# Performance work log

Hardware: AMD Instinct MI355X
Metric: run time of the kernel (lower is better)

The kernel has to match this reference:

```python
import jax, jax.numpy as jnp
import numpy as np

LRELU_GAIN = 2.0 ** 0.5  # util.lrelu_gain (assumed sqrt(2))
EPS = 1e-8


def upsample2_bilinear_ac(x):
    # F.upsample_bilinear == bilinear with align_corners=True, scale 2
    B, C, H, W = x.shape
    def lerp_axis(t, n, axis):
        c = jnp.arange(2 * n, dtype=jnp.float32) * (n - 1) / (2 * n - 1)
        i0 = jnp.floor(c).astype(jnp.int32)
        i1 = jnp.minimum(i0 + 1, n - 1)
        f = c - i0.astype(jnp.float32)
        a = jnp.take(t, i0, axis=axis)
        b = jnp.take(t, i1, axis=axis)
        shape = [1] * t.ndim
        shape[axis] = 2 * n
        f = f.reshape(shape)
        return a * (1.0 - f) + b * f
    x = lerp_axis(x, H, 2)
    x = lerp_axis(x, W, 3)
    return x


def conv1x1(x, weight, bias, gain):
    # Conv2dNormalizedLR with kernel_size=1: he = gain/sqrt(in)
    cin = weight.shape[1]
    he = gain / float(cin) ** 0.5
    y = jnp.einsum('bihw,oi->bohw', x, weight[:, :, 0, 0] * he)
    return y + bias[None, :, None, None]


def mod_conv3x3(x, weight, style, gain):
    # weight: [Cin, Cout, 3, 3]; style: [B, Cin]
    cin, cout, k, _ = weight.shape
    he = gain / float(cin * k * k) ** 0.5
    wmod = style[:, :, None, None, None] * (weight * he)[None]  # [B,Cin,Cout,k,k]
    # demodulation: normalize over (in, kh, kw) per out channel
    d = jax.lax.rsqrt(jnp.sum(wmod * wmod, axis=(1, 3, 4), keepdims=True) + EPS)
    wmod = wmod * d
    # conv_transpose2d(stride=1, pad=1, k=3) == conv2d with transposed+flipped kernel, pad=1
    kern = jnp.flip(jnp.transpose(wmod, (0, 2, 1, 3, 4)), axis=(3, 4))  # [B,Cout,Cin,k,k]
    def one(xb, kb):
        return jax.lax.conv_general_dilated(
            xb[None], kb, (1, 1), ((1, 1), (1, 1)),
            dimension_numbers=('NCHW', 'OIHW', 'NCHW'))[0]
    y = jax.vmap(one)(x, kern)
    return y * gain


def noise_affine(noise, w_s, b_s, w_b, b_b):
    # Baff*: 1x1 conv from 1 channel, gain=1 -> he=1
    ys = noise * w_s[None, :, 0, None, 0, None][:, :, :, 0] if False else noise * w_s[:, 0, 0, 0][None, :, None, None] + b_s[None, :, None, None]
    yb = noise * w_b[:, 0, 0, 0][None, :, None, None] + b_b[None, :, None, None]
    return ys, yb


def block_forward(x, w, noise1, noise2, conv1_w, bias1, conv2_w, bias2,
                  Aaff1_w, Aaff1_b, Aaff2_w, Aaff2_b,
                  Baff1s_w, Baff1s_b, Baff1b_w, Baff1b_b,
                  Baff2s_w, Baff2s_b, Baff2b_w, Baff2b_b,
                  rgb_w, rgb_b):
    x = upsample2_bilinear_ac(x)
    style1 = conv1x1(w, Aaff1_w, Aaff1_b, 1.0)[:, :, 0, 0]  # [B, Cin]
    x = mod_conv3x3(x, conv1_w, style1, LRELU_GAIN)
    ys, yb = noise_affine(noise1, Baff1s_w, Baff1s_b, Baff1b_w, Baff1b_b)
    x = x * ys + yb + bias1
    x = jax.nn.leaky_relu(x, 0.2)
    style2 = conv1x1(w, Aaff2_w, Aaff2_b, 1.0)[:, :, 0, 0]
    x = mod_conv3x3(x, conv2_w, style2, LRELU_GAIN)
    ys, yb = noise_affine(noise2, Baff2s_w, Baff2s_b, Baff2b_w, Baff2b_b)
    x = x * ys + yb + bias2
    x = jax.nn.leaky_relu(x, 0.2)
    rgb = conv1x1(x, rgb_w, rgb_b, 0.03)
    return x, rgb


def setup_inputs() -> dict:
    key = jax.random.key(0)
    ks = jax.random.split(key, 20)
    B, Cin, Cout, Wd, H, W = 8, 512, 512, 512, 32, 32
    inp = {
        'x': jax.random.normal(ks[0], (B, Cin, H, W), jnp.float32),
        'w': jax.random.normal(ks[1], (B, Wd, 1, 1), jnp.float32),
        'noise1': jax.random.normal(ks[2], (B, 1, 2 * H, 2 * W), jnp.float32),
        'noise2': jax.random.normal(ks[3], (B, 1, 2 * H, 2 * W), jnp.float32),
        'conv1_w': jax.random.normal(ks[4], (Cin, Cout, 3, 3), jnp.float32),
        'bias1': jnp.zeros((1, Cout, 1, 1), jnp.float32),
        'conv2_w': jax.random.normal(ks[5], (Cout, Cout, 3, 3), jnp.float32),
        'bias2': jnp.zeros((1, Cout, 1, 1), jnp.float32),
        'Aaff1_w': jax.random.normal(ks[6], (Cin, Wd, 1, 1), jnp.float32),
        'Aaff1_b': jnp.zeros((Cin,), jnp.float32),
        'Aaff2_w': jax.random.normal(ks[7], (Cout, Wd, 1, 1), jnp.float32),
        'Aaff2_b': jnp.zeros((Cout,), jnp.float32),
        'Baff1s_w': jax.random.normal(ks[8], (Cout, 1, 1, 1), jnp.float32) * 0.1,
        'Baff1s_b': jnp.ones((Cout,), jnp.float32),
        'Baff1b_w': jax.random.normal(ks[9], (Cout, 1, 1, 1), jnp.float32) * 0.1,
        'Baff1b_b': jnp.zeros((Cout,), jnp.float32),
        'Baff2s_w': jax.random.normal(ks[10], (Cout, 1, 1, 1), jnp.float32) * 0.1,
        'Baff2s_b': jnp.ones((Cout,), jnp.float32),
        'Baff2b_w': jax.random.normal(ks[11], (Cout, 1, 1, 1), jnp.float32) * 0.1,
        'Baff2b_b': jnp.zeros((Cout,), jnp.float32),
        'rgb_w': jax.random.normal(ks[12], (3, Cout, 1, 1), jnp.float32),
        'rgb_b': jnp.zeros((3,), jnp.float32),
    }
    return inp


def reference(x, w, noise1, noise2, conv1_w, bias1, conv2_w, bias2,
              Aaff1_w, Aaff1_b, Aaff2_w, Aaff2_b,
              Baff1s_w, Baff1s_b, Baff1b_w, Baff1b_b,
              Baff2s_w, Baff2s_b, Baff2b_w, Baff2b_b,
              rgb_w, rgb_b):
    return block_forward(x, w, noise1, noise2, conv1_w, bias1, conv2_w, bias2,
                         Aaff1_w, Aaff1_b, Aaff2_w, Aaff2_b,
                         Baff1s_w, Baff1s_b, Baff1b_w, Baff1b_b,
                         Baff2s_w, Baff2s_b, Baff2b_w, Baff2b_b,
                         rgb_w, rgb_b)
```

## Files before the change

### kernel.cpp

```cpp
#include <hip/hip_runtime.h>
#include <hip/hip_bf16.h>

#define BB 8
#define CC 512
#define HO 64
#define HP 66
#define NPIX (BB*HO*HO)

typedef float f32x4 __attribute__((ext_vector_type(4)));
typedef __bf16 bf16x8 __attribute__((ext_vector_type(8)));
using bf16 = __hip_bfloat16;

__device__ __forceinline__ void gload16(const void* g, void* l) {
    __builtin_amdgcn_global_load_lds((const __attribute__((address_space(1))) void*)g,
                                     (__attribute__((address_space(3))) void*)l, 16, 0, 0);
}

__device__ __forceinline__ float waveRedSum(float v) {
    #pragma unroll
    for (int off = 32; off; off >>= 1) v += __shfl_down(v, off);
    return v;
}

__global__ void prep_weights(const float* __restrict__ Wsrc, float* __restrict__ S2ho,
                             bf16* __restrict__ keffT, float he) {
    int t = blockIdx.x * blockDim.x + threadIdx.x;
    int i = t & (CC-1), o = t >> 9;
    const float* wp = Wsrc + (i*CC + o)*9;
    float v[9]; float s2 = 0.f;
    #pragma unroll
    for (int k = 0; k < 9; ++k) { v[k] = wp[k] * he; s2 += v[k]*v[k]; }
    S2ho[o*CC + i] = s2;
    #pragma unroll
    for (int tp = 0; tp < 9; ++tp) keffT[(tp*CC + o)*CC + i] = (bf16)v[8 - tp];
}

__global__ void style_kernel(const float* __restrict__ w,
                             const float* __restrict__ A1, const float* __restrict__ A1b,
                             const float* __restrict__ A2, const float* __restrict__ A2b,
                             float* __restrict__ s1, float* __restrict__ s2) {
    int wid = (blockIdx.x * blockDim.x + threadIdx.x) >> 6;
    int lane = threadIdx.x & 63;
    int set = wid >= BB*CC; int rem = set ? wid - BB*CC : wid;
    int b = rem >> 9, i = rem & (CC-1);
    const float* A = set ? A2 : A1;
    const float* wb = w + b*CC;
    float sum = 0.f;
    for (int d = lane; d < CC; d += 64) sum += wb[d] * A[i*CC + d];
    sum = waveRedSum(sum);
    if (lane == 0) {
        float r = sum * 0.04419417382415922f + (set ? A2b : A1b)[i];
        (set ? s2 : s1)[b*CC + i] = r;
    }
}

__global__ void demod_kernel(const float* __restrict__ s1, const float* __restrict__ S21,
                             const float* __restrict__ s2, const float* __restrict__ S22,
                             float* __restrict__ dg1, float* __restrict__ dg2, float gain) {
    int wid = (blockIdx.x * blockDim.x + threadIdx.x) >> 6;
    int lane = threadIdx.x & 63;
    int set = wid >= BB*CC; int rem = set ? wid - BB*CC : wid;
    int b = rem >> 9, o = rem & (CC-1);
    const float* st = (set ? s2 : s1) + b*CC;
    const float* S2 = (set ? S22 : S21) + o*CC;
    float sum = 0.f;
    for (int i = lane; i < CC; i += 64) { float sv = st[i]; sum += sv*sv*S2[i]; }
    sum = waveRedSum(sum);
    if (lane == 0) (set ? dg2 : dg1)[b*CC + o] = gain * rsqrtf(sum + 1e-8f);
}

__global__ void upsample_mod(const float* __restrict__ x, const float* __restrict__ s1,
                             bf16* __restrict__ xs1) {
    __shared__ float usl[16][CC];
    int blk = blockIdx.x;
    int i = threadIdx.x;
    int b = blk >> 10, rem = blk & 1023, p = rem >> 4, q0 = (rem & 15) << 2;
    const float scale = 31.0f / 63.0f;
    float chf = p * scale; int h0 = (int)chf; float fh = chf - h0; int h1 = min(h0 + 1, 31);
    int wa = min(((int)(q0 * scale)) & ~3, 24);
    const float* xb = x + ((size_t)(b*CC + i) << 10);
    f32x4 r00 = *(const f32x4*)(xb + (h0 << 5) + wa);
    f32x4 r01 = *(const f32x4*)(xb + (h0 << 5) + wa + 4);
    f32x4 r10 = *(const f32x4*)(xb + (h1 << 5) + wa);
    f32x4 r11 = *(const f32x4*)(xb + (h1 << 5) + wa + 4);
    #pragma unroll
    for (int k = 0; k < 4; ++k) {
        usl[k][i] = r00[k]; usl[4 + k][i] = r01[k];
        usl[8 + k][i] = r10[k]; usl[12 + k][i] = r11[k];
    }
    float sv = s1[b*CC + i];
    #pragma unroll
    for (int dq = 0; dq < 4; ++dq) {
        int q = q0 + dq;
        float cwf = q * scale; int w0 = (int)cwf; float fw = cwf - w0;
        int i0 = w0 - wa, i1 = min(w0 + 1, 31) - wa;
        float v00 = usl[i0][i], v01 = usl[i1][i];
        float v10 = usl[8 + i0][i], v11 = usl[8 + i1][i];
        float va = v00*(1.f-fh) + v10*fh;
        float vb = v01*(1.f-fh) + v11*fh;
        float v  = (va*(1.f-fw) + vb*fw) * sv;
        xs1[(((b*HP) + p + 1)*HP + (q + 1))*CC + i] = (bf16)v;
    }
}

__global__ void halo_zero(bf16* __restrict__ xs1, bf16* __restrict__ xs2) {
    int blk = blockIdx.x;
    bf16* dst = (blk & 1) ? xs2 : xs1;
    int idx = blk >> 1;
    int b = idx / 260, rm = idx - b*260;
    int p, q;
    if (rm < 66)       { p = 0;        q = rm; }
    else if (rm < 132) { p = 65;       q = rm - 66; }
    else if (rm < 196) { p = rm - 131; q = 0; }
    else               { p = rm - 195; q = 65; }
    f32x4* d4 = (f32x4*)(dst + ((size_t)((b*HP + p)*HP + q)) * CC);
    d4[threadIdx.x] = f32x4{0.f, 0.f, 0.f, 0.f};
}

#define SB  __builtin_amdgcn_sched_barrier(0)
#define BAR __builtin_amdgcn_s_barrier()
#define VMC(n)  asm volatile("s_waitcnt vmcnt(" #n ")" ::: "memory")
#define LGKM(n) asm volatile("s_waitcnt lgkmcnt(" #n ")" ::: "memory")

#define STAGE_A(d, h, U) do { \
    gload16((U) + aThr + (h)*(HP*1024),                 ldsA + (d)*32768 + (h)*16384); \
    gload16((U) + aThr + (h)*(HP*1024) + 2*(HP*1024),   ldsA + (d)*32768 + (h)*16384 + 8192); \
} while (0)

#define STAGE_B(d, h, U) do { \
    gload16((U) + bThr + (h)*32768,                     ldsB + (d)*32768 + (h)*16384); \
    gload16((U) + bThr + (h)*32768 + 131072,            ldsB + (d)*32768 + (h)*16384 + 8192); \
} while (0)

#define LOAD_A(d, fh) do { \
    _Pragma("unroll") \
    for (int fmq = 0; fmq < 4; ++fmq) { \
        afr[fmq][0] = *(const bf16x8*)(aRd + (d)*32768 + (fh)*16384 + fmq*2048 + swz0); \
        afr[fmq][1] = *(const bf16x8*)(aRd + (d)*32768 + (fh)*16384 + fmq*2048 + swz1); \
    } } while (0)

#define LOAD_B(d, nh) do { \
    _Pragma("unroll") \
    for (int fnq = 0; fnq < 2; ++fnq) { \
        bfr[nh][fnq][0] = *(const bf16x8*)(bRd + (d)*32768 + (nh)*16384 + fnq*2048 + swz0); \
        bfr[nh][fnq][1] = *(const bf16x8*)(bRd + (d)*32768 + (nh)*16384 + fnq*2048 + swz1); \
    } } while (0)

#define QUAD(fh, nh) do { \
    __builtin_amdgcn_s_setprio(1); \
    _Pragma("unroll") \
    for (int kc = 0; kc < 2; ++kc) \
    { _Pragma("unroll") \
      for (int fmq = 0; fmq < 4; ++fmq) \
      { _Pragma("unroll") \
        for (int fnq = 0; fnq < 2; ++fnq) \
            acc[(fh)*4+fmq][(nh)*2+fnq] = __builtin_amdgcn_mfma_f32_16x16x32_bf16( \
                afr[fmq][kc], bfr[nh][fnq][kc], acc[(fh)*4+fmq][(nh)*2+fnq], 0, 0, 0); } } \
    __builtin_amdgcn_s_setprio(0); } while (0)

#define PHSTEP(cur, nxt, aN1, bN1, aN2, g1, g3) do { \
     \
    LOAD_A(cur, 0); \
    LOAD_B(cur, 0); \
    if (g1) STAGE_B(nxt, 0, bN1); \
    LGKM(8); SB; BAR; LGKM(0); SB; \
    QUAD(0, 0); \
    VMC(4); SB; BAR; SB; \
     \
    LOAD_B(cur, 1); \
    if (g1) STAGE_B(nxt, 1, bN1); \
    SB; BAR; LGKM(0); SB; \
    QUAD(0, 1); \
    SB; BAR; SB; \
     \
    LOAD_A(cur, 1); \
    if (g1) STAGE_A(nxt, 1, aN1); \
    SB; BAR; LGKM(0); SB; \
    QUAD(1, 1); \
    SB; BAR; SB; \
     \
    if (g3) STAGE_A(cur, 0, aN2); \
    SB; BAR; SB; \
    QUAD(1, 0); \
    if (g3) { VMC(6); } else { VMC(0); } \
    SB; BAR; SB; \
} while (0)

template<int PHASE>
__global__ __launch_bounds__(512, 2) void conv_gemm(
    const bf16* __restrict__ xs, const bf16* __restrict__ keffT,
    const float* __restrict__ dg, const float* __restrict__ noise,
    const float* __restrict__ nsw, const float* __restrict__ nsb,
    const float* __restrict__ nbw, const float* __restrict__ nbb,
    const float* __restrict__ biasv, const float* __restrict__ stnext,
    bf16* __restrict__ outb, float* __restrict__ outf) {
    __shared__ __attribute__((aligned(16))) bf16 As[32768];
    __shared__ __attribute__((aligned(16))) bf16 Bs[32768];
    const int tid = threadIdx.x;
    const int wave = tid >> 6, lane = tid & 63;
    const int tileId = ((blockIdx.x & 7) << 5) + (blockIdx.x >> 3);
    const int mtile = tileId >> 1, ntile = tileId & 1;
    const int m0 = mtile << 8, n0 = ntile << 8;
    const int b  = m0 >> 12;
    const int p0 = (m0 & 4095) >> 6;
    const int wm = wave >> 2, wn = wave & 3;
    const int l15 = lane & 15;

    const int srcSwz = (((tid & 7) ^ ((tid >> 3) & 7)) << 4);
    const int aThr = ((tid >> 3) << 10) + srcSwz;
    const int bThr = (((tid >> 8) & 1) << 16) + (((tid >> 3) & 31) << 10) + srcSwz;
    char* const ldsA = (char*)As + tid*16;
    char* const ldsB = (char*)Bs + tid*16;

    const char* const aRd = (const char*)As + (((wm << 6) + l15) << 7);
    const char* const bRd = (const char*)Bs + (((wn << 5) + l15) << 7);
    const int swz0 = (((lane >> 4)    ) ^ (lane & 7)) << 4;
    const int swz1 = (((lane >> 4) | 4) ^ (lane & 7)) << 4;

    f32x4 acc[8][4];
    #pragma unroll
    for (int i_ = 0; i_ < 8; ++i_)
        #pragma unroll
        for (int j_ = 0; j_ < 4; ++j_) acc[i_][j_] = f32x4{0.f, 0.f, 0.f, 0.f};
    bf16x8 afr[4][2], bfr[2][2][2];

    auto abase = [&](int st) -> const char* {
        int t = st >> 3; int dh = (t*11) >> 5; int dw = t - dh*3;
        return (const char*)xs + ((size_t)((b*HP + p0 + dh)*HP + dw) << 10) + ((st & 7) << 7);
    };
    auto bbase = [&](int st) -> const char* {
        int t = st >> 3;
        return (const char*)keffT + ((size_t)(t*CC + n0) << 10) + ((st & 7) << 7);
    };

    {
        const char* a0 = abase(0); const char* b0 = bbase(0); const char* a1 = abase(1);
        STAGE_A(0, 0, a0);
        STAGE_B(0, 0, b0);
        STAGE_B(0, 1, b0);
        STAGE_A(0, 1, a0);
        STAGE_A(1, 0, a1);
        VMC(6); SB; BAR; SB;
    }

    #pragma unroll 1
    for (int it = 0; it < 36; ++it) {
        const bool more = (it < 35);
        const char* aE = abase(2*it + 1); const char* bE = bbase(2*it + 1);
        const char* aO = abase(2*it + 2); const char* bO = bbase(2*it + 2);
        const char* aO2 = abase(2*it + 3);
        PHSTEP(0, 1, aE, bE, aO,  true, more);
        PHSTEP(1, 0, aO, bO, aO2, more, more);
    }

    const float* dgb = dg + b*CC;
    int nIdx[4]; float pdg[4], pnsw[4], pnsb[4], pnbw[4], pnbb[4], pbias[4], pst[4];
    #pragma unroll
    for (int fn = 0; fn < 4; ++fn) {
        int n = n0 + (wn << 6) + (fn << 4) + l15;
        nIdx[fn] = n;
        pdg[fn] = dgb[n]; pnsw[fn] = nsw[n]; pnsb[fn] = nsb[n];
        pnbw[fn] = nbw[n]; pnbb[fn] = nbb[n]; pbias[fn] = biasv[n];
        if (PHASE == 1) pst[fn] = stnext[b*CC + n]; else pst[fn] = 0.f;
    }
    #pragma unroll
    for (int fm = 0; fm < 8; ++fm) {
        const int mbase = m0 + (wm << 7) + (fm << 4) + ((lane >> 4) << 2);
        const f32x4 nsv = *(const f32x4*)(noise + mbase);
        if (PHASE == 2) {
            #pragma unroll
            for (int fn = 0; fn < 4; ++fn) {
                f32x4 vv;
                #pragma unroll
                for (int r = 0; r < 4; ++r) {
                    float ns = nsv[r];
                    float v = acc[fm][fn][r] * pdg[fn];
                    v = v * (ns*pnsw[fn] + pnsb[fn]) + (ns*pnbw[fn] + pnbb[fn]) + pbias[fn];
                    vv[r] = fmaxf(v, 0.2f*v);
                }
                *(f32x4*)(outf + ((size_t)(b*CC + nIdx[fn]) << 12) + (mbase & 4095)) = vv;
            }
        } else {
            #pragma unroll
            for (int r = 0; r < 4; ++r) {
                int mloc = mbase + r;
                float ns = nsv[r];
                int prow = (mloc & 4095) >> 6, qcol = mloc & 63;
                #pragma unroll
                for (int fn = 0; fn < 4; ++fn) {
                    float v = acc[fm][fn][r] * pdg[fn];
                    v = v * (ns*pnsw[fn] + pnsb[fn]) + (ns*pnbw[fn] + pnbb[fn]) + pbias[fn];
                    v = fmaxf(v, 0.2f*v);
                    outb[(((b*HP) + prow + 1)*HP + (qcol + 1))*CC + nIdx[fn]] =
                        (bf16)(v * pst[fn]);
                }
            }
        }
    }
}

__global__ void rgb_kernel(const float* __restrict__ xf, const float* __restrict__ rgbw,
                           const float* __restrict__ rgbb, float* __restrict__ out) {
    __shared__ float red[3][4][64];
    int tid = threadIdx.x;
    int wv = tid >> 6, ln = tid & 63;
    int pix = blockIdx.x * 64 + ln;
    int b = pix >> 12, rem = pix & 4095;
    const float* xb = xf + (((size_t)b*CC) << 12) + rem;
    float a0 = 0.f, a1 = 0.f, a2 = 0.f;
    int o0 = wv << 7;
    #pragma unroll 8
    for (int o = o0; o < o0 + 128; ++o) {
        float xv = xb[(size_t)o << 12];
        a0 += xv * rgbw[o]; a1 += xv * rgbw[CC+o]; a2 += xv * rgbw[2*CC+o];
    }
    red[0][wv][ln] = a0; red[1][wv][ln] = a1; red[2][wv][ln] = a2;
    __syncthreads();
    if (wv == 0) {
        const float he = 0.03f * 0.04419417382415922f;
        #pragma unroll
        for (int c = 0; c < 3; ++c) {
            float s = red[c][0][ln] + red[c][1][ln] + red[c][2][ln] + red[c][3][ln];
            out[(b*3+c)*4096 + rem] = s*he + rgbb[c];
        }
    }
}

extern "C" void kernel_launch(void* const* d_in, const int* in_sizes, int n_in,
                              void* d_out, int out_size, void* d_ws, size_t ws_size,
                              hipStream_t stream) {
    const float* x      = (const float*)d_in[0];
    const float* w      = (const float*)d_in[1];
    const float* noise1 = (const float*)d_in[2];
    const float* noise2 = (const float*)d_in[3];
    const float* conv1w = (const float*)d_in[4];
    const float* bias1  = (const float*)d_in[5];
    const float* conv2w = (const float*)d_in[6];
    const float* bias2  = (const float*)d_in[7];
    const float* A1w = (const float*)d_in[8];
    const float* A1b = (const float*)d_in[9];
    const float* A2w = (const float*)d_in[10];
    const float* A2b = (const float*)d_in[11];
    const float* B1sw = (const float*)d_in[12];
    const float* B1sb = (const float*)d_in[13];
    const float* B1bw = (const float*)d_in[14];
    const float* B1bb = (const float*)d_in[15];
    const float* B2sw = (const float*)d_in[16];
    const float* B2sb = (const float*)d_in[17];
    const float* B2bw = (const float*)d_in[18];
    const float* B2bb = (const float*)d_in[19];
    const float* rgbw = (const float*)d_in[20];
    const float* rgbb = (const float*)d_in[21];

    char* ws = (char*)d_ws;
    size_t off = 0;
    auto alloc = [&](size_t bytes) { char* p = ws + off; off += (bytes + 255) & ~(size_t)255; return p; };
    const size_t xsBytes = (size_t)BB*HP*HP*CC*2;
    bf16* xs1 = (bf16*)alloc(xsBytes);
    bf16* xs2 = (bf16*)alloc(xsBytes);
    bf16* kT1 = (bf16*)alloc((size_t)9*CC*CC*2);
    bf16* kT2 = (bf16*)alloc((size_t)9*CC*CC*2);
    float* S21 = (float*)alloc((size_t)CC*CC*4);
    float* S22 = (float*)alloc((size_t)CC*CC*4);
    float* s1  = (float*)alloc(BB*CC*4);
    float* s2  = (float*)alloc(BB*CC*4);
    float* dg1 = (float*)alloc(BB*CC*4);
    float* dg2 = (float*)alloc(BB*CC*4);

    float* outx   = (float*)d_out;
    float* outrgb = outx + (size_t)BB*CC*HO*HO;

    const float gain = 1.41421356237309515f;
    const float he = gain / sqrtf(512.f * 9.f);
    halo_zero<<<4160, 64, 0, stream>>>(xs1, xs2);
    prep_weights<<<CC*CC/256, 256, 0, stream>>>(conv1w, S21, kT1, he);
    prep_weights<<<CC*CC/256, 256, 0, stream>>>(conv2w, S22, kT2, he);
    style_kernel<<<2*BB*CC/4, 256, 0, stream>>>(w, A1w, A1b, A2w, A2b, s1, s2);
    demod_kernel<<<2*BB*CC/4, 256, 0, stream>>>(s1, S21, s2, S22, dg1, dg2, gain);
    upsample_mod<<<BB*HO*16, CC, 0, stream>>>(x, s1, xs1);
    conv_gemm<1><<<(NPIX/256)*(CC/256), 512, 0, stream>>>(
        xs1, kT1, dg1, noise1, B1sw, B1sb, B1bw, B1bb, bias1, s2, xs2, nullptr);
    conv_gemm<2><<<(NPIX/256)*(CC/256), 512, 0, stream>>>(
        xs2, kT2, dg2, noise2, B2sw, B2sb, B2bw, B2bb, bias2, nullptr, nullptr, outx);
    rgb_kernel<<<NPIX/64, 256, 0, stream>>>(outx, rgbw, rgbb, outrgb);
}
```

Before: 356.4 us.

## Fuse toRGB projection into conv2 epilogue and vectorize conv1 bf16 stores

Removes the standalone rgb_kernel. The conv2 epilogue now computes per-pixel partial RGB sums in registers, reduces them across lanes with shuffles, and accumulates them into an output pre-initialized with the bias using atomicAdd. Separately, conv1 swaps the MFMA operand order so each lane holds four consecutive channels, which lets the epilogue write packed 8-byte bf16 stores instead of scattered 2-byte ones. The cost is float atomics, which make the summation order nondeterministic, plus an extra init kernel.

```diff
diff --git a/kernel.cpp b/kernel.cpp
--- a/kernel.cpp
+++ b/kernel.cpp
@@ -117,6 +117,13 @@
     d4[threadIdx.x] = f32x4{0.f, 0.f, 0.f, 0.f};
 }
 
+__global__ void rgb_init(const float* __restrict__ rgbb, float* __restrict__ outrgb) {
+    int t = blockIdx.x * blockDim.x + threadIdx.x;
+    int plane = t >> 10, c = plane - (plane/3)*3;
+    float v = rgbb[c];
+    *(f32x4*)(outrgb + (plane << 12) + ((t & 1023) << 2)) = f32x4{v, v, v, v};
+}
+
 #define SB  __builtin_amdgcn_sched_barrier(0)
 #define BAR __builtin_amdgcn_s_barrier()
 #define VMC(n)  asm volatile("s_waitcnt vmcnt(" #n ")" ::: "memory")
@@ -153,9 +160,14 @@
     { _Pragma("unroll") \
       for (int fmq = 0; fmq < 4; ++fmq) \
       { _Pragma("unroll") \
-        for (int fnq = 0; fnq < 2; ++fnq) \
-            acc[(fh)*4+fmq][(nh)*2+fnq] = __builtin_amdgcn_mfma_f32_16x16x32_bf16( \
-                afr[fmq][kc], bfr[nh][fnq][kc], acc[(fh)*4+fmq][(nh)*2+fnq], 0, 0, 0); } } \
+        for (int fnq = 0; fnq < 2; ++fnq) { \
+            if (PHASE == 1) \
+                acc[(fh)*4+fmq][(nh)*2+fnq] = __builtin_amdgcn_mfma_f32_16x16x32_bf16( \
+                    bfr[nh][fnq][kc], afr[fmq][kc], acc[(fh)*4+fmq][(nh)*2+fnq], 0, 0, 0); \
+            else \
+                acc[(fh)*4+fmq][(nh)*2+fnq] = __builtin_amdgcn_mfma_f32_16x16x32_bf16( \
+                    afr[fmq][kc], bfr[nh][fnq][kc], acc[(fh)*4+fmq][(nh)*2+fnq], 0, 0, 0); \
+        } } } \
     __builtin_amdgcn_s_setprio(0); } while (0)
 
 #define PHSTEP(cur, nxt, aN1, bN1, aN2, g1, g3) do { \
@@ -193,7 +205,8 @@
     const float* __restrict__ nsw, const float* __restrict__ nsb,
     const float* __restrict__ nbw, const float* __restrict__ nbb,
     const float* __restrict__ biasv, const float* __restrict__ stnext,
-    bf16* __restrict__ outb, float* __restrict__ outf) {
+    bf16* __restrict__ outb, float* __restrict__ outf,
+    const float* __restrict__ rgbwv, float* __restrict__ outrgb) {
     __shared__ __attribute__((aligned(16))) bf16 As[32768];
     __shared__ __attribute__((aligned(16))) bf16 Bs[32768];
     const int tid = threadIdx.x;
@@ -253,21 +266,60 @@
         PHSTEP(1, 0, aO, bO, aO2, more, more);
     }
 
-    const float* dgb = dg + b*CC;
-    int nIdx[4]; float pdg[4], pnsw[4], pnsb[4], pnbw[4], pnbb[4], pbias[4], pst[4];
-    #pragma unroll
-    for (int fn = 0; fn < 4; ++fn) {
-        int n = n0 + (wn << 6) + (fn << 4) + l15;
-        nIdx[fn] = n;
-        pdg[fn] = dgb[n]; pnsw[fn] = nsw[n]; pnsb[fn] = nsb[n];
-        pnbw[fn] = nbw[n]; pnbb[fn] = nbb[n]; pbias[fn] = biasv[n];
-        if (PHASE == 1) pst[fn] = stnext[b*CC + n]; else pst[fn] = 0.f;
-    }
-    #pragma unroll
-    for (int fm = 0; fm < 8; ++fm) {
-        const int mbase = m0 + (wm << 7) + (fm << 4) + ((lane >> 4) << 2);
-        const f32x4 nsv = *(const f32x4*)(noise + mbase);
-        if (PHASE == 2) {
+    if constexpr (PHASE == 1) {
+        const int chq = (lane >> 4) << 2;
+        float ns8[8]; int pox[8];
+        #pragma unroll
+        for (int fm = 0; fm < 8; ++fm) {
+            int mloc = m0 + (wm << 7) + (fm << 4) + l15;
+            ns8[fm] = noise[mloc];
+            int prow = (mloc & 4095) >> 6, qcol = mloc & 63;
+            pox[fm] = ((b*HP + prow + 1)*HP + (qcol + 1))*CC;
+        }
+        #pragma unroll
+        for (int fn = 0; fn < 4; ++fn) {
+            const int cb = n0 + (wn << 6) + (fn << 4) + chq;
+            f32x4 dg4 = *(const f32x4*)(dg + b*CC + cb);
+            f32x4 sw4 = *(const f32x4*)(nsw + cb);
+            f32x4 sb4 = *(const f32x4*)(nsb + cb);
+            f32x4 bw4 = *(const f32x4*)(nbw + cb);
+            f32x4 bb4 = *(const f32x4*)(nbb + cb);
+            f32x4 bi4 = *(const f32x4*)(biasv + cb);
+            f32x4 st4 = *(const f32x4*)(stnext + b*CC + cb);
+            #pragma unroll
+            for (int fm = 0; fm < 8; ++fm) {
+                float ns = ns8[fm];
+                union { bf16 h[4]; uint2 u; } pk;
+                #pragma unroll
+                for (int r = 0; r < 4; ++r) {
+                    float v = acc[fm][fn][r] * dg4[r];
+                    v = v * (ns*sw4[r] + sb4[r]) + (ns*bw4[r] + bb4[r]) + bi4[r];
+                    v = fmaxf(v, 0.2f*v);
+                    pk.h[r] = (bf16)(v * st4[r]);
+                }
+                *(uint2*)(outb + pox[fm] + cb) = pk.u;
+            }
+        }
+    } else {
+        const float* dgb = dg + b*CC;
+        int nIdx[4]; float pdg[4], pnsw[4], pnsb[4], pnbw[4], pnbb[4], pbias[4];
+        float w0[4], w1[4], w2[4];
+        const float heR = 0.03f * 0.04419417382415922f;
+        #pragma unroll
+        for (int fn = 0; fn < 4; ++fn) {
+            int n = n0 + (wn << 6) + (fn << 4) + l15;
+            nIdx[fn] = n;
+            pdg[fn] = dgb[n]; pnsw[fn] = nsw[n]; pnsb[fn] = nsb[n];
+            pnbw[fn] = nbw[n]; pnbb[fn] = nbb[n]; pbias[fn] = biasv[n];
+            w0[fn] = rgbwv[n] * heR;
+            w1[fn] = rgbwv[CC + n] * heR;
+            w2[fn] = rgbwv[2*CC + n] * heR;
+        }
+        #pragma unroll
+        for (int fm = 0; fm < 8; ++fm) {
+            const int mbase = m0 + (wm << 7) + (fm << 4) + ((lane >> 4) << 2);
+            const f32x4 nsv = *(const f32x4*)(noise + mbase);
+            f32x4 pc0 = {0.f,0.f,0.f,0.f}, pc1 = {0.f,0.f,0.f,0.f}, pc2 = {0.f,0.f,0.f,0.f};
             #pragma unroll
             for (int fn = 0; fn < 4; ++fn) {
                 f32x4 vv;
@@ -278,50 +330,25 @@
                     v = v * (ns*pnsw[fn] + pnsb[fn]) + (ns*pnbw[fn] + pnbb[fn]) + pbias[fn];
                     vv[r] = fmaxf(v, 0.2f*v);
                 }
+                pc0 += vv * w0[fn]; pc1 += vv * w1[fn]; pc2 += vv * w2[fn];
                 *(f32x4*)(outf + ((size_t)(b*CC + nIdx[fn]) << 12) + (mbase & 4095)) = vv;
             }
-        } else {
             #pragma unroll
             for (int r = 0; r < 4; ++r) {
-                int mloc = mbase + r;
-                float ns = nsv[r];
-                int prow = (mloc & 4095) >> 6, qcol = mloc & 63;
+                float a0 = pc0[r], a1 = pc1[r], a2 = pc2[r];
                 #pragma unroll
-                for (int fn = 0; fn < 4; ++fn) {
-                    float v = acc[fm][fn][r] * pdg[fn];
-                    v = v * (ns*pnsw[fn] + pnsb[fn]) + (ns*pnbw[fn] + pnbb[fn]) + pbias[fn];
-                    v = fmaxf(v, 0.2f*v);
-                    outb[(((b*HP) + prow + 1)*HP + (qcol + 1))*CC + nIdx[fn]] =
-                        (bf16)(v * pst[fn]);
+                for (int mk = 1; mk < 16; mk <<= 1) {
+                    a0 += __shfl_xor(a0, mk);
+                    a1 += __shfl_xor(a1, mk);
+                    a2 += __shfl_xor(a2, mk);
+                }
+                if (l15 == 0) {
+                    int px = (mbase + r) & 4095;
+                    atomicAdd(outrgb + (b*3 + 0)*4096 + px, a0);
+                    atomicAdd(outrgb + (b*3 + 1)*4096 + px, a1);
+                    atomicAdd(outrgb + (b*3 + 2)*4096 + px, a2);
                 }
             }
-        }
-    }
-}
-
-__global__ void rgb_kernel(const float* __restrict__ xf, const float* __restrict__ rgbw,
-                           const float* __restrict__ rgbb, float* __restrict__ out) {
-    __shared__ float red[3][4][64];
-    int tid = threadIdx.x;
-    int wv = tid >> 6, ln = tid & 63;
-    int pix = blockIdx.x * 64 + ln;
-    int b = pix >> 12, rem = pix & 4095;
-    const float* xb = xf + (((size_t)b*CC) << 12) + rem;
-    float a0 = 0.f, a1 = 0.f, a2 = 0.f;
-    int o0 = wv << 7;
-    #pragma unroll 8
-    for (int o = o0; o < o0 + 128; ++o) {
-        float xv = xb[(size_t)o << 12];
-        a0 += xv * rgbw[o]; a1 += xv * rgbw[CC+o]; a2 += xv * rgbw[2*CC+o];
-    }
-    red[0][wv][ln] = a0; red[1][wv][ln] = a1; red[2][wv][ln] = a2;
-    __syncthreads();
-    if (wv == 0) {
-        const float he = 0.03f * 0.04419417382415922f;
-        #pragma unroll
-        for (int c = 0; c < 3; ++c) {
-            float s = red[c][0][ln] + red[c][1][ln] + red[c][2][ln] + red[c][3][ln];
-            out[(b*3+c)*4096 + rem] = s*he + rgbb[c];
         }
     }
 }
@@ -373,14 +400,16 @@
     const float gain = 1.41421356237309515f;
     const float he = gain / sqrtf(512.f * 9.f);
     halo_zero<<<4160, 64, 0, stream>>>(xs1, xs2);
+    rgb_init<<<96, 256, 0, stream>>>(rgbb, outrgb);
     prep_weights<<<CC*CC/256, 256, 0, stream>>>(conv1w, S21, kT1, he);
     prep_weights<<<CC*CC/256, 256, 0, stream>>>(conv2w, S22, kT2, he);
     style_kernel<<<2*BB*CC/4, 256, 0, stream>>>(w, A1w, A1b, A2w, A2b, s1, s2);
     demod_kernel<<<2*BB*CC/4, 256, 0, stream>>>(s1, S21, s2, S22, dg1, dg2, gain);
     upsample_mod<<<BB*HO*16, CC, 0, stream>>>(x, s1, xs1);
     conv_gemm<1><<<(NPIX/256)*(CC/256), 512, 0, stream>>>(
-        xs1, kT1, dg1, noise1, B1sw, B1sb, B1bw, B1bb, bias1, s2, xs2, nullptr);
+        xs1, kT1, dg1, noise1, B1sw, B1sb, B1bw, B1bb, bias1, s2, xs2, nullptr,
+        nullptr, nullptr);
     conv_gemm<2><<<(NPIX/256)*(CC/256), 512, 0, stream>>>(
-        xs2, kT2, dg2, noise2, B2sw, B2sb, B2bw, B2bb, bias2, nullptr, nullptr, outx);
-    rgb_kernel<<<NPIX/64, 256, 0, stream>>>(outx, rgbw, rgbb, outrgb);
-}
+        xs2, kT2, dg2, noise2, B2sw, B2sb, B2bw, B2bb, bias2, nullptr, nullptr, outx,
+        rgbw, outrgb);
+}
```

After: 359.3 us. About the same (+0.8%).
